# Kernel optimization log

Hardware: AMD Instinct MI355X
Metric: run time of the kernel (lower is better)

Reference implementation:

```python
import jax, jax.numpy as jnp
import numpy as np
from jax import lax

B, A, T, D, V, K = 16, 1024, 512, 256, 50000, 3
EXP_DILS = [1, 2, 4, 8, 16, 32, 32]  # conv_num=7, exp_num=5
REF_DILS = [1, 1, 1]                 # refine_num=3


def setup_inputs() -> dict:
    key = jax.random.key(0)
    ks = jax.random.split(key, 14)
    inp = {
        'article_word': jax.random.randint(ks[0], (B, A), 0, V),
        'article_char': jax.random.randint(ks[1], (B, A, 16), 0, 100),
        'template_word': jax.random.randint(ks[2], (B, T), 0, V),
        'template_char': jax.random.randint(ks[3], (B, T, 16), 0, 100),
        'article_mask': jnp.ones((B, A), jnp.float32),
        'template_mask': jnp.ones((B, T), jnp.float32),
        'emb': jax.random.normal(ks[4], (V, D), jnp.float32) * 0.02,
        'exp_w': jax.random.normal(ks[5], (7, K, D, 2 * D), jnp.float32) * 0.03,
        'exp_b': jnp.zeros((7, 2 * D), jnp.float32),
        'ref_w': jax.random.normal(ks[6], (3, K, D, 2 * D), jnp.float32) * 0.03,
        'ref_b': jnp.zeros((3, 2 * D), jnp.float32),
        'ff1_w': jax.random.normal(ks[7], (10, 10), jnp.float32) * 0.3,
        'ff1_b': jnp.zeros((10,), jnp.float32),
        'ff2_w': jax.random.normal(ks[8], (10, 1), jnp.float32) * 0.3,
        'ff2_b': jnp.zeros((1,), jnp.float32),
    }
    return inp


def _res_block(x, w, b, dilation):
    # x: [B, L, D]; w: [K, D, 2D]  (Conv1d, padding='same' given k//2*dilation)
    pad = (K // 2) * dilation
    y = lax.conv_general_dilated(x, w, window_strides=(1,), padding=[(pad, pad)],
                                 rhs_dilation=(dilation,),
                                 dimension_numbers=('NWC', 'WIO', 'NWC')) + b
    a, g = jnp.split(y, 2, axis=2)  # GLU on channel dim
    return x + a * jax.nn.sigmoid(g)


def _encode(x, exp_w, exp_b, ref_w, ref_b):
    for i, d in enumerate(EXP_DILS):
        x = _res_block(x, exp_w[i], exp_b[i], d)
    for i, d in enumerate(REF_DILS):
        x = _res_block(x, ref_w[i], ref_b[i], d)
    return x  # dropout is identity in eval mode


def reference(article_word, article_char, template_word, template_char,
              article_mask, template_mask, emb, exp_w, exp_b, ref_w, ref_b,
              ff1_w, ff1_b, ff2_w, ff2_b):
    art = _encode(emb[article_word], exp_w, exp_b, ref_w, ref_b)    # [B,A,D]
    tpl = _encode(emb[template_word], exp_w, exp_b, ref_w, ref_b)   # [B,T,D]
    # pairwise squared distance without materializing [B,A,T,D]
    a2 = jnp.sum(art * art, axis=-1)                 # [B,A]
    t2 = jnp.sum(tpl * tpl, axis=-1)                 # [B,T]
    dot = jnp.einsum('bad,btd->bat', art, tpl)       # [B,A,T]
    dist = jnp.maximum(a2[:, :, None] + t2[:, None, :] - 2.0 * dot, 0.0)
    S = jnp.exp(-dist) * article_mask[:, :, None] * template_mask[:, None, :]
    row_max = jnp.max(S, axis=2)                     # [B,A]
    top, _ = lax.top_k(row_max, 10)                  # sorted descending, [B,10]
    h = jax.nn.relu(top @ ff1_w + ff1_b)             # [B,10]
    out = (h @ ff2_w + ff2_b).squeeze()              # [B]
    return out
```

## Files before the change

kernel.cpp:

```cpp
#include <hip/hip_runtime.h>
#include <math.h>

#define NB 16
#define NA 1024
#define NT 512
#define ND 256
#define PAD 32

typedef short bf8_t __attribute__((ext_vector_type(8)));
typedef float f4_t __attribute__((ext_vector_type(4)));

__device__ __forceinline__ float bf2f(ushort u) {
    union { unsigned int i; float f; } v; v.i = ((unsigned int)u) << 16; return v.f;
}
__device__ __forceinline__ ushort f2bf(float f) {
    union { float f; unsigned int i; } v; v.f = f;
    unsigned int x = v.i;
    unsigned int r = (x + 0x7fffu + ((x >> 16) & 1u)) >> 16;
    return (ushort)r;
}
__device__ __forceinline__ void gl_lds16(const void* g, void* l) {
    __builtin_amdgcn_global_load_lds(
        (const __attribute__((address_space(1))) unsigned int*)g,
        (__attribute__((address_space(3))) unsigned int*)l, 16, 0, 0);
}


__global__ void __launch_bounds__(256)
setup_kernel(const int* __restrict__ art_w, const int* __restrict__ tpl_w,
             const float* __restrict__ emb,
             ushort* __restrict__ art_a, ushort* __restrict__ art_b,
             ushort* __restrict__ tpl_a, ushort* __restrict__ tpl_b,
             const float* __restrict__ exp_w, const float* __restrict__ ref_w,
             ushort* __restrict__ wpack,
             float* __restrict__ a2, float* __restrict__ t2) {
    __shared__ float tile[64][65];
    int bid = blockIdx.x;
    int tid = threadIdx.x;

    if (bid < 2048) {
        int idx = bid * 256 + tid;
        int l = idx & (NA - 1);
        int bq = idx >> 10;
        int qq = bq & 31, b = bq >> 5;
        int wd = art_w[b * NA + l];
        const float4* src = (const float4*)(emb + (size_t)wd * ND + qq * 8);
        float4 v0 = src[0], v1 = src[1];
        ushort o[8];
        o[0]=f2bf(v0.x); o[1]=f2bf(v0.y); o[2]=f2bf(v0.z); o[3]=f2bf(v0.w);
        o[4]=f2bf(v1.x); o[5]=f2bf(v1.y); o[6]=f2bf(v1.z); o[7]=f2bf(v1.w);
        *(uint4*)(art_a + ((size_t)bq * (NA + 64) + PAD + l) * 8) = *(uint4*)o;
        return;
    }
    bid -= 2048;
    if (bid < 1024) {
        int j = bid * 256 + tid;
        int l = j & (NT - 1);
        int bq = j >> 9;
        int qq = bq & 31, b = bq >> 5;
        int wd = tpl_w[b * NT + l];
        const float4* src = (const float4*)(emb + (size_t)wd * ND + qq * 8);
        float4 v0 = src[0], v1 = src[1];
        ushort o[8];
        o[0]=f2bf(v0.x); o[1]=f2bf(v0.y); o[2]=f2bf(v0.z); o[3]=f2bf(v0.w);
        o[4]=f2bf(v1.x); o[5]=f2bf(v1.y); o[6]=f2bf(v1.z); o[7]=f2bf(v1.w);
        *(uint4*)(tpl_a + ((size_t)bq * (NT + 64) + PAD + l) * 8) = *(uint4*)o;
        return;
    }
    bid -= 1024;
    if (bid < 512) {
        int j = bid * 256 + tid;
        int y = j >> 15;
        int rem = j & 32767;
        ushort* p = (y == 0) ? art_a : (y == 1) ? art_b : (y == 2) ? tpl_a : tpl_b;
        int L = (y < 2) ? NA : NT;
        int Lp = L + 2 * PAD;
        int plane = rem >> 6;
        int row_in = rem & 63;
        int slab = (row_in < PAD) ? row_in : L + row_in;
        uint4 z = make_uint4(0, 0, 0, 0);
        *(uint4*)(p + ((size_t)plane * Lp + slab) * 8) = z;
        return;
    }
    bid -= 512;
    if (bid < 24) {
        int i = (bid * 256 + tid) * 4;
        float4 z = make_float4(0.f, 0.f, 0.f, 0.f);
        if (i < NB * NA) *(float4*)(a2 + i) = z;
        else             *(float4*)(t2 + i - NB * NA) = z;
        return;
    }
    bid -= 24;
    {
        int li = bid / 96;
        int r = bid % 96;
        int gk = r >> 3;
        int gc = r & 7;
        const float* src = (li < 7) ? exp_w + (size_t)li * 3 * ND * 512
                                    : ref_w + (size_t)(li - 7) * 3 * ND * 512;
        int k0g = gk * 64, c0 = gc * 64;
        #pragma unroll
        for (int p = 0; p < 4; ++p) {
            int kr = p * 16 + (tid >> 4);
            int cc = (tid & 15) * 4;
            *(float4*)&tile[kr][cc] =
                *(const float4*)(src + (size_t)(k0g + kr) * 512 + c0 + cc);
        }
        __syncthreads();
        int tap = k0g >> 8, kl0 = k0g & 255, kc0 = kl0 >> 5;
        int ag = c0 >> 8, cb = (c0 & 255) >> 6;
        int kg = tid >> 5, idx = tid & 31;
        int kc = kc0 + (kg >> 2), qq = kg & 3;
        #pragma unroll
        for (int h = 0; h < 2; ++h) {
            int w64 = idx + h * 32;
            int cprime = h * 64 + ag * 32 + idx;
            ushort o[8];
            #pragma unroll
            for (int j = 0; j < 8; ++j) o[j] = f2bf(tile[kg * 8 + j][w64]);
            ushort* d = wpack +
                (((((size_t)(li * 4 + cb) * 3 + tap) * 8 + kc) * 4 + qq) * 128 + cprime) * 8;
            *(uint4*)d = *(uint4*)o;
        }
    }
}

__global__ void __launch_bounds__(256, 4)
conv_glu_mfma(const ushort* __restrict__ art_x, ushort* __restrict__ art_y,
              const ushort* __restrict__ tpl_x, ushort* __restrict__ tpl_y,
              const ushort* __restrict__ wp, const float* __restrict__ bias,
              int dil, int last, float* __restrict__ a2, float* __restrict__ t2) {
    __shared__ char smem[34816];
    ushort* Als = (ushort*)smem;
    float* ylds = (float*)smem;

    const int tid = threadIdx.x;
    const int w = tid >> 6, lane = tid & 63;
    const int wm = w >> 1, wn = w & 1;
    const int q = lane >> 4, l15 = lane & 15;

    const int id = blockIdx.x;
    const int cb = (id >> 3) & 3;
    const int pb = ((id >> 5) << 3) | (id & 7);
    const int plane = pb % 12;
    const int b = pb / 12;
    const int b32 = b * 32;

    int Lp, l0;
    const ushort* xb;
    ushort* yb;
    float* sq;
    int sqbase;
    if (plane < 8) {
        Lp = NA + 2 * PAD; l0 = plane * 128;
        xb = art_x; yb = art_y; sq = a2; sqbase = b * NA + l0;
    } else {
        Lp = NT + 2 * PAD; l0 = (plane - 8) * 128;
        xb = tpl_x; yb = tpl_y; sq = t2; sqbase = b * NT + l0;
    }
    const ushort* wl = wp + (size_t)cb * 98304;
    const int boff = (q * 128 + wn * 64 + l15) * 8;

    f4_t acc[4][4];
    #pragma unroll
    for (int i = 0; i < 4; ++i)
        #pragma unroll
        for (int j = 0; j < 4; ++j)
            acc[i][j] = (f4_t){0.f, 0.f, 0.f, 0.f};

    for (int kc2 = 0; kc2 < 4; ++kc2) {
        #pragma unroll
        for (int s3 = 0; s3 < 6; ++s3) {
            int s = w + s3 * 4;
            int h = s / 12, within = s % 12;
            int qq = kc2 * 8 + h * 4 + within / 3;
            int rphys = l0 + (within % 3) * 64 + lane;
            gl_lds16(xb + ((size_t)(b32 + qq) * Lp + rphys) * 8, Als + s * 512);
        }
        __syncthreads();

        #pragma unroll
        for (int h = 0; h < 2; ++h) {
            const int kc = kc2 * 2 + h;
            const ushort* wkc = wl + kc * 4096 + boff;
            const ushort* Ah = Als + h * 6144;
            #pragma unroll
            for (int t = 0; t < 3; ++t) {
                bf8_t bfr[4];
                #pragma unroll
                for (int nt = 0; nt < 4; ++nt)
                    bfr[nt] = *(const bf8_t*)(wkc + t * 32768 + nt * 128);
                const int sh = (t - 1) * dil;
                bf8_t af[4];
                #pragma unroll
                for (int mt = 0; mt < 4; ++mt)
                    af[mt] = *(const bf8_t*)(Ah + (q * 192 + 32 + sh + wm * 64 + mt * 16 + l15) * 8);
                #pragma unroll
                for (int mt = 0; mt < 4; ++mt)
                    #pragma unroll
                    for (int nt = 0; nt < 4; ++nt)
                        acc[mt][nt] = __builtin_amdgcn_mfma_f32_16x16x32_bf16(
                            af[mt], bfr[nt], acc[mt][nt], 0, 0, 0);
            }
        }
        __syncthreads();
    }

    #pragma unroll
    for (int nt = 0; nt < 2; ++nt) {
        const int cl = wn * 32 + nt * 16 + l15;
        const int chan = cb * 64 + cl;
        const float ba = bias[chan];
        const float bg2 = bias[chan + 256];
        #pragma unroll
        for (int mt = 0; mt < 4; ++mt) {
            #pragma unroll
            for (int r = 0; r < 4; ++r) {
                const int row = wm * 64 + mt * 16 + q * 4 + r;
                float av = acc[mt][nt][r] + ba;
                float gv = acc[mt][nt + 2][r] + bg2;
                ylds[row * 68 + cl] = av / (1.f + __expf(-gv));
            }
        }
    }
    __syncthreads();

    float ss = 0.f;
    #pragma unroll
    for (int p = 0; p < 4; ++p) {
        int u = p * 256 + tid;
        int cl8 = u >> 7;
        int row = u & 127;
        size_t go = ((size_t)(b32 + cb * 8 + cl8) * Lp + l0 + PAD + row) * 8;
        ushort xv[8]; *(uint4*)xv = *(const uint4*)(xb + go);
        float4 y0 = *(float4*)&ylds[row * 68 + cl8 * 8];
        float4 y1 = *(float4*)&ylds[row * 68 + cl8 * 8 + 4];
        ushort ov[8];
        ov[0]=f2bf(bf2f(xv[0])+y0.x); ov[1]=f2bf(bf2f(xv[1])+y0.y);
        ov[2]=f2bf(bf2f(xv[2])+y0.z); ov[3]=f2bf(bf2f(xv[3])+y0.w);
        ov[4]=f2bf(bf2f(xv[4])+y1.x); ov[5]=f2bf(bf2f(xv[5])+y1.y);
        ov[6]=f2bf(bf2f(xv[6])+y1.z); ov[7]=f2bf(bf2f(xv[7])+y1.w);
        *(uint4*)(yb + go) = *(uint4*)ov;
        if (last) {
            #pragma unroll
            for (int j = 0; j < 8; ++j) { float f = bf2f(ov[j]); ss += f * f; }
        }
    }
    if (last) {
        float* ssred = (float*)smem;
        __syncthreads();
        ssred[tid] = ss;
        __syncthreads();
        if (tid < 128)
            atomicAdd(&sq[sqbase + tid], ssred[tid] + ssred[tid + 128]);
    }
}

__global__ void __launch_bounds__(256, 4)
dist_rowmax_mfma(const ushort* __restrict__ art, const ushort* __restrict__ tpl,
                 const float* __restrict__ a2, const float* __restrict__ t2,
                 const float* __restrict__ amask, const float* __restrict__ tmask,
                 float* __restrict__ rmaxp) {
    __shared__ ushort Als[64 * 32];
    __shared__ ushort Bls[128 * 32];
    __shared__ float red[2][64];

    const int tid = threadIdx.x;
    const int w = tid >> 6, lane = tid & 63;
    const int wm = w >> 1, wn = w & 1;
    const int q = lane >> 4, l15 = lane & 15;

    const int id = blockIdx.x;
    const int b = (id & 7) | (((id >> 3) & 1) << 3);
    const int rest = id >> 4;
    const int a0 = (rest & 15) * 64;
    const int tplane = rest >> 4;
    const int t0 = tplane * 128;
    const int b32 = b * 32;
    const int LpA = NA + 2 * PAD, LpT = NT + 2 * PAD;

    float a2v[2][4], amv[2][4];
    #pragma unroll
    for (int mt = 0; mt < 2; ++mt)
        #pragma unroll
        for (int r = 0; r < 4; ++r) {
            int row = a0 + wm * 32 + mt * 16 + q * 4 + r;
            a2v[mt][r] = a2[b * NA + row];
            amv[mt][r] = amask[b * NA + row];
        }

    f4_t acc[2][4];
    #pragma unroll
    for (int i = 0; i < 2; ++i)
        #pragma unroll
        for (int j = 0; j < 4; ++j)
            acc[i][j] = (f4_t){0.f, 0.f, 0.f, 0.f};

    for (int kb = 0; kb < 8; ++kb) {
        #pragma unroll
        for (int s3 = 0; s3 < 3; ++s3) {
            int s = w + s3 * 4;
            if (s < 4) {
                int qq = kb * 4 + s;
                gl_lds16(art + ((size_t)(b32 + qq) * LpA + PAD + a0 + lane) * 8,
                         Als + s * 512);
            } else {
                int s2 = s - 4;
                int qq = kb * 4 + (s2 >> 1);
                int r0 = (s2 & 1) * 64;
                gl_lds16(tpl + ((size_t)(b32 + qq) * LpT + PAD + t0 + r0 + lane) * 8,
                         Bls + s2 * 512);
            }
        }
        __syncthreads();

        bf8_t af[2], bfr[4];
        #pragma unroll
        for (int mt = 0; mt < 2; ++mt)
            af[mt] = *(const bf8_t*)(Als + (q * 64 + wm * 32 + mt * 16 + l15) * 8);
        #pragma unroll
        for (int nt = 0; nt < 4; ++nt)
            bfr[nt] = *(const bf8_t*)(Bls + (q * 128 + wn * 64 + nt * 16 + l15) * 8);
        #pragma unroll
        for (int mt = 0; mt < 2; ++mt)
            #pragma unroll
            for (int nt = 0; nt < 4; ++nt)
                acc[mt][nt] = __builtin_amdgcn_mfma_f32_16x16x32_bf16(
                    af[mt], bfr[nt], acc[mt][nt], 0, 0, 0);
        __syncthreads();
    }

    float rm[2][4];
    #pragma unroll
    for (int mt = 0; mt < 2; ++mt)
        #pragma unroll
        for (int r = 0; r < 4; ++r) rm[mt][r] = 0.f;

    #pragma unroll
    for (int nt = 0; nt < 4; ++nt) {
        int t = t0 + wn * 64 + nt * 16 + l15;
        float t2v = t2[b * NT + t];
        float tmv = tmask[b * NT + t];
        #pragma unroll
        for (int mt = 0; mt < 2; ++mt)
            #pragma unroll
            for (int r = 0; r < 4; ++r) {
                float d = a2v[mt][r] + t2v - 2.f * acc[mt][nt][r];
                d = fmaxf(d, 0.f);
                float s = __expf(-d) * amv[mt][r] * tmv;
                rm[mt][r] = fmaxf(rm[mt][r], s);
            }
    }
    #pragma unroll
    for (int mt = 0; mt < 2; ++mt)
        #pragma unroll
        for (int r = 0; r < 4; ++r) {
            float v = rm[mt][r];
            #pragma unroll
            for (int off = 1; off < 16; off <<= 1)
                v = fmaxf(v, __shfl_xor(v, off));
            rm[mt][r] = v;
        }
    if (l15 == 0) {
        #pragma unroll
        for (int mt = 0; mt < 2; ++mt)
            #pragma unroll
            for (int r = 0; r < 4; ++r)
                red[wn][wm * 32 + mt * 16 + q * 4 + r] = rm[mt][r];
    }
    __syncthreads();
    if (tid < 64)
        rmaxp[((size_t)tplane * NB + b) * NA + a0 + tid] =
            fmaxf(red[0][tid], red[1][tid]);
}

__global__ void __launch_bounds__(256)
topk_mlp_kernel(const float* __restrict__ rmaxp,
                const float* __restrict__ ff1_w, const float* __restrict__ ff1_b,
                const float* __restrict__ ff2_w, const float* __restrict__ ff2_b,
                float* __restrict__ out) {
    __shared__ float vals[NA];
    __shared__ float top[10];
    __shared__ float h[10];
    __shared__ float rv[4];
    __shared__ int ri[4];

    int b = blockIdx.x;
    int tid = threadIdx.x;
    int lane = tid & 63, wv = tid >> 6;
    for (int i = tid; i < NA; i += 256) {
        float m = rmaxp[(size_t)b * NA + i];
        m = fmaxf(m, rmaxp[((size_t)NB + b) * NA + i]);
        m = fmaxf(m, rmaxp[((size_t)2 * NB + b) * NA + i]);
        m = fmaxf(m, rmaxp[((size_t)3 * NB + b) * NA + i]);
        vals[i] = m;
    }
    __syncthreads();

    for (int it = 0; it < 10; ++it) {
        float best = -1e30f;
        int bi = 0;
        #pragma unroll
        for (int u = 0; u < 4; ++u) {
            int i = u * 256 + tid;
            if (vals[i] > best) { best = vals[i]; bi = i; }
        }
        #pragma unroll
        for (int off = 32; off; off >>= 1) {
            float ob = __shfl_down(best, off);
            int oi = __shfl_down(bi, off);
            if (ob > best) { best = ob; bi = oi; }
        }
        if (lane == 0) { rv[wv] = best; ri[wv] = bi; }
        __syncthreads();
        if (tid == 0) {
            float bb = rv[0]; int bbi = ri[0];
            #pragma unroll
            for (int k = 1; k < 4; ++k)
                if (rv[k] > bb) { bb = rv[k]; bbi = ri[k]; }
            top[it] = bb; vals[bbi] = -1e30f;
        }
        __syncthreads();
    }

    if (tid < 10) {
        float s = ff1_b[tid];
        #pragma unroll
        for (int i = 0; i < 10; ++i) s += top[i] * ff1_w[i * 10 + tid];
        h[tid] = fmaxf(s, 0.f);
    }
    __syncthreads();
    if (tid == 0) {
        float s = ff2_b[0];
        #pragma unroll
        for (int j = 0; j < 10; ++j) s += h[j] * ff2_w[j];
        out[b] = s;
    }
}

extern "C" void kernel_launch(void* const* d_in, const int* in_sizes, int n_in,
                              void* d_out, int out_size, void* d_ws, size_t ws_size,
                              hipStream_t stream) {
    const int*   art_w = (const int*)d_in[0];
    const int*   tpl_w = (const int*)d_in[2];
    const float* amask = (const float*)d_in[4];
    const float* tmask = (const float*)d_in[5];
    const float* emb   = (const float*)d_in[6];
    const float* exp_w = (const float*)d_in[7];
    const float* exp_b = (const float*)d_in[8];
    const float* ref_w = (const float*)d_in[9];
    const float* ref_b = (const float*)d_in[10];
    const float* ff1_w = (const float*)d_in[11];
    const float* ff1_b = (const float*)d_in[12];
    const float* ff2_w = (const float*)d_in[13];
    const float* ff2_b = (const float*)d_in[14];
    float* out = (float*)d_out;

    const size_t art_bytes = (size_t)NB * 32 * (NA + 2 * PAD) * 8 * 2;
    const size_t tpl_bytes = (size_t)NB * 32 * (NT + 2 * PAD) * 8 * 2;
    const size_t wpk_bytes = (size_t)10 * 4 * 3 * 8 * 4 * 128 * 8 * 2;

    char* p = (char*)d_ws;
    ushort* art_a = (ushort*)p; p += art_bytes;
    ushort* art_b = (ushort*)p; p += art_bytes;
    ushort* tpl_a = (ushort*)p; p += tpl_bytes;
    ushort* tpl_b = (ushort*)p; p += tpl_bytes;
    ushort* wpack = (ushort*)p; p += wpk_bytes;
    float* a2    = (float*)p; p += (size_t)NB * NA * 4;
    float* t2    = (float*)p; p += (size_t)NB * NT * 4;
    float* rmaxp = (float*)p; p += (size_t)4 * NB * NA * 4;

    setup_kernel<<<4568, 256, 0, stream>>>(art_w, tpl_w, emb,
                                           art_a, art_b, tpl_a, tpl_b,
                                           exp_w, ref_w, wpack, a2, t2);

    const int dils[10] = {1, 2, 4, 8, 16, 32, 32, 1, 1, 1};

    ushort* a_cur = art_a; ushort* a_nxt = art_b;
    ushort* t_cur = tpl_a; ushort* t_nxt = tpl_b;
    for (int i = 0; i < 10; ++i) {
        const ushort* wl = wpack + (size_t)i * 4 * 98304;
        const float* bb = (i < 7) ? exp_b + (size_t)i * 512
                                  : ref_b + (size_t)(i - 7) * 512;
        conv_glu_mfma<<<768, 256, 0, stream>>>(
            a_cur, a_nxt, t_cur, t_nxt, wl, bb, dils[i], (i == 9) ? 1 : 0, a2, t2);
        ushort* t1 = a_cur; a_cur = a_nxt; a_nxt = t1;
        ushort* t2p = t_cur; t_cur = t_nxt; t_nxt = t2p;
    }
    ushort* art_fin = a_cur;
    ushort* tpl_fin = t_cur;

    dist_rowmax_mfma<<<1024, 256, 0, stream>>>(
        art_fin, tpl_fin, a2, t2, amask, tmask, rmaxp);

    topk_mlp_kernel<<<NB, 256, 0, stream>>>(rmaxp, ff1_w, ff1_b, ff2_w, ff2_b, out);
}
```

Before: 374.8 us.

## Load conv activations directly from global into registers instead of staging through LDS

The conv GLU kernel no longer stages activation tiles into shared memory with async global-to-LDS loads and barriers. Each wave now reads its A fragments for all three taps straight from global memory into registers, alongside the weight fragments, then issues all MFMAs per K chunk. The launch bound is relaxed to 2 blocks per SU to make room for the larger register set. This removes LDS traffic and block syncs, but overlapping taps now reload the same rows from global/L2 per wave, and occupancy may drop.

```diff
diff --git a/kernel.cpp b/kernel.cpp
--- a/kernel.cpp
+++ b/kernel.cpp
@@ -125,14 +125,12 @@
     }
 }
 
-__global__ void __launch_bounds__(256, 4)
+__global__ void __launch_bounds__(256, 2)
 conv_glu_mfma(const ushort* __restrict__ art_x, ushort* __restrict__ art_y,
               const ushort* __restrict__ tpl_x, ushort* __restrict__ tpl_y,
               const ushort* __restrict__ wp, const float* __restrict__ bias,
               int dil, int last, float* __restrict__ a2, float* __restrict__ t2) {
-    __shared__ char smem[34816];
-    ushort* Als = (ushort*)smem;
-    float* ylds = (float*)smem;
+    __shared__ float ylds[128 * 68];
 
     const int tid = threadIdx.x;
     const int w = tid >> 6, lane = tid & 63;
@@ -160,6 +158,7 @@
     }
     const ushort* wl = wp + (size_t)cb * 98304;
     const int boff = (q * 128 + wn * 64 + l15) * 8;
+    const int arowoff = l0 + PAD + wm * 64 + l15;
 
     f4_t acc[4][4];
     #pragma unroll
@@ -168,42 +167,28 @@
         for (int j = 0; j < 4; ++j)
             acc[i][j] = (f4_t){0.f, 0.f, 0.f, 0.f};
 
-    for (int kc2 = 0; kc2 < 4; ++kc2) {
-        #pragma unroll
-        for (int s3 = 0; s3 < 6; ++s3) {
-            int s = w + s3 * 4;
-            int h = s / 12, within = s % 12;
-            int qq = kc2 * 8 + h * 4 + within / 3;
-            int rphys = l0 + (within % 3) * 64 + lane;
-            gl_lds16(xb + ((size_t)(b32 + qq) * Lp + rphys) * 8, Als + s * 512);
-        }
-        __syncthreads();
-
-        #pragma unroll
-        for (int h = 0; h < 2; ++h) {
-            const int kc = kc2 * 2 + h;
-            const ushort* wkc = wl + kc * 4096 + boff;
-            const ushort* Ah = Als + h * 6144;
-            #pragma unroll
-            for (int t = 0; t < 3; ++t) {
-                bf8_t bfr[4];
+    for (int kc = 0; kc < 8; ++kc) {
+        const ushort* wkc = wl + kc * 4096 + boff;
+        const ushort* abase = xb + ((size_t)(b32 + kc * 4 + q) * Lp + arowoff) * 8;
+        bf8_t af[3][4], bfr[3][4];
+        #pragma unroll
+        for (int t = 0; t < 3; ++t) {
+            const int sh = (t - 1) * dil;
+            #pragma unroll
+            for (int mt = 0; mt < 4; ++mt)
+                af[t][mt] = *(const bf8_t*)(abase + (sh + mt * 16) * 8);
+            #pragma unroll
+            for (int nt = 0; nt < 4; ++nt)
+                bfr[t][nt] = *(const bf8_t*)(wkc + t * 32768 + nt * 128);
+        }
+        #pragma unroll
+        for (int t = 0; t < 3; ++t)
+            #pragma unroll
+            for (int mt = 0; mt < 4; ++mt)
                 #pragma unroll
                 for (int nt = 0; nt < 4; ++nt)
-                    bfr[nt] = *(const bf8_t*)(wkc + t * 32768 + nt * 128);
-                const int sh = (t - 1) * dil;
-                bf8_t af[4];
-                #pragma unroll
-                for (int mt = 0; mt < 4; ++mt)
-                    af[mt] = *(const bf8_t*)(Ah + (q * 192 + 32 + sh + wm * 64 + mt * 16 + l15) * 8);
-                #pragma unroll
-                for (int mt = 0; mt < 4; ++mt)
-                    #pragma unroll
-                    for (int nt = 0; nt < 4; ++nt)
-                        acc[mt][nt] = __builtin_amdgcn_mfma_f32_16x16x32_bf16(
-                            af[mt], bfr[nt], acc[mt][nt], 0, 0, 0);
-            }
-        }
-        __syncthreads();
+                    acc[mt][nt] = __builtin_amdgcn_mfma_f32_16x16x32_bf16(
+                        af[t][mt], bfr[t][nt], acc[mt][nt], 0, 0, 0);
     }
 
     #pragma unroll
@@ -247,7 +232,7 @@
         }
     }
     if (last) {
-        float* ssred = (float*)smem;
+        float* ssred = (float*)ylds;
         __syncthreads();
         ssred[tid] = ss;
         __syncthreads();
```

Measured after the change: 596.3 us. +59.1%, slower.
